# Performance work log

Hardware: AMD Instinct MI355X
Metric: run time of the kernel (lower is better)

The kernel has to match this reference:

```python
import jax, jax.numpy as jnp
import numpy as np
from jax import lax

VOCAB = 18
EMB = 200
HID = 200
SEQ = 128
BATCH = 2048
PAD_IDX = 0


def setup_inputs() -> dict:
    key = jax.random.key(0)
    ks = jax.random.split(key, 8)
    s_emb = 1.0  # torch nn.Embedding default N(0,1)
    s_lstm = 1.0 / np.sqrt(HID)  # torch LSTM default U(-1/sqrt(H), 1/sqrt(H))
    s_lin = 1.0 / np.sqrt(HID)
    inp = {
        "x": jax.random.randint(ks[0], (BATCH, SEQ), 0, VOCAB, dtype=jnp.int32),
        "E": jax.random.normal(ks[1], (VOCAB, EMB), dtype=jnp.float32) * s_emb,
        "W_ih": jax.random.uniform(ks[2], (4 * HID, EMB), minval=-s_lstm, maxval=s_lstm, dtype=jnp.float32),
        "W_hh": jax.random.uniform(ks[3], (4 * HID, HID), minval=-s_lstm, maxval=s_lstm, dtype=jnp.float32),
        "b_ih": jax.random.uniform(ks[4], (4 * HID,), minval=-s_lstm, maxval=s_lstm, dtype=jnp.float32),
        "b_hh": jax.random.uniform(ks[5], (4 * HID,), minval=-s_lstm, maxval=s_lstm, dtype=jnp.float32),
        "W_out": jax.random.uniform(ks[6], (VOCAB, HID), minval=-s_lin, maxval=s_lin, dtype=jnp.float32),
        "b_out": jax.random.uniform(ks[7], (VOCAB,), minval=-s_lin, maxval=s_lin, dtype=jnp.float32),
    }
    return inp


def _forward(x, E, W_ih, W_hh, b_ih, b_hh, W_out, b_out):
    # Embedding with padding_idx=0 (row 0 is zero, no grad flows to it)
    pad_mask = (jnp.arange(VOCAB) != PAD_IDX).astype(E.dtype)[:, None]
    emb = (E * pad_mask)[x]  # (B, T, EMB)
    B = emb.shape[0]
    # Precompute input contribution to all gates for every timestep
    x_proj = jnp.einsum("bte,ge->btg", emb, W_ih) + b_ih + b_hh  # (B, T, 4H)

    def step(carry, xg_t):
        h, c = carry
        gates = xg_t + h @ W_hh.T  # (B, 4H)
        i, f, g, o = jnp.split(gates, 4, axis=-1)  # torch gate order i,f,g,o
        i = jax.nn.sigmoid(i)
        f = jax.nn.sigmoid(f)
        g = jnp.tanh(g)
        o = jax.nn.sigmoid(o)
        c = f * c + i * g
        h = o * jnp.tanh(c)
        return (h, c), h

    h0 = jnp.zeros((B, HID), dtype=emb.dtype)
    c0 = jnp.zeros((B, HID), dtype=emb.dtype)
    (h_n, c_n), hs = lax.scan(step, (h0, c0), x_proj.transpose(1, 0, 2))
    out = hs.transpose(1, 0, 2)  # (B, T, HID)
    logits = out @ W_out.T + b_out  # (B, T, VOCAB)
    return logits, h_n, c_n


def reference(x, E, W_ih, W_hh, b_ih, b_hh, W_out, b_out):
    return _forward(x, E, W_ih, W_hh, b_ih, b_hh, W_out, b_out)
```

## Files before the change

kernel.cpp:

```cpp
#include <hip/hip_runtime.h>

#define VOCAB 18
#define EMB   200
#define HID   200
#define G4    800
#define SEQ   128
#define BATCH 2048
#define MB    8
#define NT    56
#define KS    7
#define TPB   256
#define TPW   14
#define SV    (SEQ*VOCAB)
#define LOGITS_N ((size_t)BATCH*SEQ*VOCAB)

typedef short s16x8 __attribute__((ext_vector_type(8)));
typedef float f32x4 __attribute__((ext_vector_type(4)));

__device__ __forceinline__ unsigned short f2bf(float f) {
  unsigned int u = __float_as_uint(f);
  u += 0x7FFFu + ((u >> 16) & 1u);
  return (unsigned short)(u >> 16);
}
__device__ __forceinline__ float sigm(float x) {
  float e = __builtin_amdgcn_exp2f(x * 1.4426950408889634f);
  return e * __builtin_amdgcn_rcpf(e + 1.0f);
}
__device__ __forceinline__ float tanhq(float x) {
  float e = __builtin_amdgcn_exp2f(x * 2.8853900817779268f);
  return 1.0f - 2.0f * __builtin_amdgcn_rcpf(e + 1.0f);
}

__global__ void prep_tbl(const float* __restrict__ E, const float* __restrict__ W_ih,
                         const float* __restrict__ b_ih, const float* __restrict__ b_hh,
                         unsigned short* __restrict__ tbl) {
  int tid = blockIdx.x * 256 + threadIdx.x;
  if (tid >= VOCAB * G4) return;
  int v = tid / G4, col = tid % G4;
  float s = b_ih[col] + b_hh[col];
  if (v != 0) {
    const float* Er = E + v * EMB;
    const float* Wr = W_ih + col * EMB;
    for (int e = 0; e < EMB; ++e) s += Er[e] * Wr[e];
  }
  tbl[tid] = f2bf(s);
}

__global__ void prep_wp(const float* __restrict__ W_hh, const float* __restrict__ W_out,
                        const float* __restrict__ b_out,
                        const unsigned short* __restrict__ tbl,
                        short* __restrict__ Wp) {
  int u = blockIdx.x * 256 + threadIdx.x;
  if (u >= NT * KS * 64) return;
  int n    = u / (KS * 64);
  int rem  = u % (KS * 64);
  int s_   = rem >> 6;
  int lane = rem & 63;
  int c    = lane & 15;
  int kb   = lane >> 4;
  s16x8 o;
  #pragma unroll
  for (int i = 0; i < 8; ++i) {
    int k = 32 * s_ + 8 * kb + i;
    short b = 0;
    if (n < 50) {
      int g = c & 3, j = 4 * n + (c >> 2);
      int colg = g * 200 + j;
      if (k < HID)                          b = (short)f2bf(W_hh[colg * HID + k]);
      else if (k >= 201 && k < 201 + VOCAB) b = (short)tbl[(k - 201) * G4 + colg];
    } else if (n < 52) {
      int v = 16 * (n - 50) + c;
      if (v < VOCAB) {
        if (k < HID)       b = (short)f2bf(W_out[v * HID + k]);
        else if (k == HID) b = (short)f2bf(b_out[v]);
      }
    }
    o[i] = b;
  }
  *(s16x8*)(Wp + (size_t)u * 8) = o;
}

__global__ __launch_bounds__(TPB) __attribute__((amdgpu_waves_per_eu(1, 1)))
void lstm_kernel(const int* __restrict__ x, const short* __restrict__ Wp,
                 float* __restrict__ out) {
  __shared__ unsigned short hA[KS * 64 * 8];
  __shared__ int   xtok[MB * SEQ];
  __shared__ float logL[MB * SV];
  __shared__ float scr[4][2][8 * 36];

  const int tid  = threadIdx.x;
  const int lane = tid & 63;
  const int w    = tid >> 6;
  const int blk  = blockIdx.x;

  const int wbase = (lane >> 4) * 144 + ((lane & 15) >> 2) * 4 + (lane & 3);
  const int rbase = (lane >> 3) * 36 + (lane & 7) * 4;
  const int jw = 56 * w;

  for (int i = tid; i < KS * 64 * 8; i += TPB)
    hA[i] = (i >= 3200 && i < 3264 && (i & 7) == 0) ? (unsigned short)0x3F80
                                                    : (unsigned short)0;
  for (int i = tid; i < MB * SEQ; i += TPB) xtok[i] = x[blk * (MB * SEQ) + i];

  s16x8 wf[TPW][KS];
  #pragma unroll
  for (int n = 0; n < TPW; ++n) {
    #pragma unroll
    for (int s = 0; s < KS; ++s) {
      wf[n][s] = *(const s16x8*)(Wp + ((((w * TPW + n) * KS) + s) * 64 + lane) * 8);
      asm volatile("" : "+a"(wf[n][s]));
    }
    asm volatile("" ::: "memory");
  }

  float creg[7] = {0.f, 0.f, 0.f, 0.f, 0.f, 0.f, 0.f};
  __syncthreads();

#define DO_PAIR(P, CC) {                                                          \
    f32x4 aA = {0.f,0.f,0.f,0.f}, aB = {0.f,0.f,0.f,0.f};                         \
    _Pragma("unroll")                                                             \
    for (int s = 0; s < KS; ++s) {                                                \
      aA = __builtin_amdgcn_mfma_f32_16x16x32_bf16(aF[s], wf[2*(P)][s],   aA, 0,0,0); \
      aB = __builtin_amdgcn_mfma_f32_16x16x32_bf16(aF[s], wf[2*(P)+1][s], aB, 0,0,0); \
    }                                                                             \
    float* sc = &scr[w][(P) & 1][0];                                              \
    if (lane < 32) {                                                              \
      float* sw = sc + wbase;                                                     \
      sw[0]  = aA[0]; sw[36] = aA[1]; sw[72] = aA[2]; sw[108] = aA[3];            \
      sw[16] = aB[0]; sw[52] = aB[1]; sw[88] = aB[2]; sw[124] = aB[3];            \
    }                                                                             \
    f32x4 gt = *(const f32x4*)(sc + rbase);                                       \
    float i_ = sigm(gt[0]);                                                       \
    float f_ = sigm(gt[1]);                                                       \
    float g_ = tanhq(gt[2]);                                                      \
    float o_ = sigm(gt[3]);                                                       \
    float cn = f_ * (CC) + i_ * g_;                                               \
    float h  = o_ * tanhq(cn);                                                    \
    (CC) = cn;                                                                    \
    int j = jw + 8 * (P) + (lane & 7);                                            \
    hA[((j >> 5) * 64 + 16 * ((j >> 3) & 3) + (lane >> 3)) * 8 + (j & 7)] = f2bf(h); \
    if (t == SEQ - 1) {                                                           \
      size_t bg = (size_t)blk * MB + (lane >> 3);                                 \
      out[LOGITS_N + bg * HID + j] = h;                                           \
      out[LOGITS_N + (size_t)BATCH * HID + bg * HID + j] = cn;                    \
    }                                                                             \
  }

  #pragma unroll 1
  for (int t = 0; t < SEQ; ++t) {
    s16x8 aF[KS];
    #pragma unroll
    for (int s = 0; s < KS; ++s) aF[s] = *(const s16x8*)&hA[(s * 64 + lane) * 8];
    {
      int vv = xtok[(lane & 7) * SEQ + t];
      int js = (lane & 8) ? 100 : (vv + 9 - 8 * (lane >> 4));
      s16x8 a6 = aF[6];
      #pragma unroll
      for (int e = 0; e < 8; ++e)
        a6[e] = (e == js) ? (short)0x3F80 : a6[e];
      aF[6] = a6;
    }

    if (w < 3) {
      DO_PAIR(0, creg[0]); DO_PAIR(1, creg[1]); DO_PAIR(2, creg[2]);
      DO_PAIR(3, creg[3]); DO_PAIR(4, creg[4]); DO_PAIR(5, creg[5]);
      DO_PAIR(6, creg[6]);
    } else {
      DO_PAIR(0, creg[0]); DO_PAIR(1, creg[1]);
      DO_PAIR(2, creg[2]); DO_PAIR(3, creg[3]);
      f32x4 a1 = {0.f,0.f,0.f,0.f}, a2 = {0.f,0.f,0.f,0.f};
      #pragma unroll
      for (int s = 0; s < KS; ++s) {
        a1 = __builtin_amdgcn_mfma_f32_16x16x32_bf16(aF[s], wf[8][s], a1, 0, 0, 0);
        a2 = __builtin_amdgcn_mfma_f32_16x16x32_bf16(aF[s], wf[9][s], a2, 0, 0, 0);
      }
      if (t > 0 && lane < 32) {
        int qrow = (lane >> 4) * 4, c = lane & 15;
        #pragma unroll
        for (int q = 0; q < 4; ++q) {
          if (c < VOCAB)      logL[(qrow + q) * SV + (t - 1) * VOCAB + c]      = a1[q];
          if (c < VOCAB - 16) logL[(qrow + q) * SV + (t - 1) * VOCAB + 16 + c] = a2[q];
        }
      }
    }
    __syncthreads();
  }

  if (w == 3) {
    s16x8 aE[KS];
    #pragma unroll
    for (int s = 0; s < KS; ++s) aE[s] = *(const s16x8*)&hA[(s * 64 + lane) * 8];
    f32x4 a1 = {0.f,0.f,0.f,0.f}, a2 = {0.f,0.f,0.f,0.f};
    #pragma unroll
    for (int s = 0; s < KS; ++s) {
      a1 = __builtin_amdgcn_mfma_f32_16x16x32_bf16(aE[s], wf[8][s], a1, 0, 0, 0);
      a2 = __builtin_amdgcn_mfma_f32_16x16x32_bf16(aE[s], wf[9][s], a2, 0, 0, 0);
    }
    if (lane < 32) {
      int qrow = (lane >> 4) * 4, c = lane & 15;
      #pragma unroll
      for (int q = 0; q < 4; ++q) {
        int base = (qrow + q) * SV + (SEQ - 1) * VOCAB;
        if (c < VOCAB)      logL[base + c]      = a1[q];
        if (c < VOCAB - 16) logL[base + 16 + c] = a2[q];
      }
    }
  }
  __syncthreads();

  float* dst = out + (size_t)blk * (MB * SV);
  for (int i = tid * 4; i < MB * SV; i += TPB * 4)
    *(f32x4*)&dst[i] = *(const f32x4*)&logL[i];
#undef DO_PAIR
}

extern "C" void kernel_launch(void* const* d_in, const int* in_sizes, int n_in,
                              void* d_out, int out_size, void* d_ws, size_t ws_size,
                              hipStream_t stream) {
  const int*   x     = (const int*)  d_in[0];
  const float* E     = (const float*)d_in[1];
  const float* W_ih  = (const float*)d_in[2];
  const float* W_hh  = (const float*)d_in[3];
  const float* b_ih  = (const float*)d_in[4];
  const float* b_hh  = (const float*)d_in[5];
  const float* W_out = (const float*)d_in[6];
  const float* b_out = (const float*)d_in[7];
  float* out = (float*)d_out;

  unsigned short* tbl = (unsigned short*)d_ws;
  short* Wp = (short*)d_ws + VOCAB * G4;

  prep_tbl<<<(VOCAB * G4 + 255) / 256, 256, 0, stream>>>(E, W_ih, b_ih, b_hh, tbl);
  prep_wp<<<(NT * KS * 64 + 255) / 256, 256, 0, stream>>>(W_hh, W_out, b_out, tbl, Wp);
  lstm_kernel<<<BATCH / MB, TPB, 0, stream>>>(x, Wp, out);
}
```

Measured before the change: 354.8 us.

## Replace LDS gate transpose with DPP shuffles and software-pipeline MFMA with elementwise

Drops the per-pair shared-memory scratch round trip used to regroup the four gate values, and instead does a 4x4 register transpose with DPP quad-permute moves. The MFMA tile pairs are software-pipelined so the next pair's matrix multiplies are issued before the current pair's sigmoid/tanh work. A barrier is added after the hA fragment load so h can be overwritten in the same step. This costs more live accumulator registers and an extra barrier per step, and only half the lanes do the elementwise work.

```diff
diff --git a/kernel.cpp b/kernel.cpp
--- a/kernel.cpp
+++ b/kernel.cpp
@@ -29,6 +29,14 @@
 __device__ __forceinline__ float tanhq(float x) {
   float e = __builtin_amdgcn_exp2f(x * 2.8853900817779268f);
   return 1.0f - 2.0f * __builtin_amdgcn_rcpf(e + 1.0f);
+}
+__device__ __forceinline__ float dpp_x1(float v) {
+  return __uint_as_float((unsigned)__builtin_amdgcn_mov_dpp(
+      (int)__float_as_uint(v), 0xB1, 0xF, 0xF, true));
+}
+__device__ __forceinline__ float dpp_x2(float v) {
+  return __uint_as_float((unsigned)__builtin_amdgcn_mov_dpp(
+      (int)__float_as_uint(v), 0x4E, 0xF, 0xF, true));
 }
 
 __global__ void prep_tbl(const float* __restrict__ E, const float* __restrict__ W_ih,
@@ -86,16 +94,15 @@
   __shared__ unsigned short hA[KS * 64 * 8];
   __shared__ int   xtok[MB * SEQ];
   __shared__ float logL[MB * SV];
-  __shared__ float scr[4][2][8 * 36];
 
   const int tid  = threadIdx.x;
   const int lane = tid & 63;
   const int w    = tid >> 6;
   const int blk  = blockIdx.x;
-
-  const int wbase = (lane >> 4) * 144 + ((lane & 15) >> 2) * 4 + (lane & 3);
-  const int rbase = (lane >> 3) * 36 + (lane & 7) * 4;
-  const int jw = 56 * w;
+  const int jw   = 56 * w;
+  const int jj   = (lane >> 2) & 3;
+  const int row  = 4 * ((lane >> 4) & 3) + (lane & 3);
+  const bool pb0 = lane & 1, pb1 = lane & 2;
 
   for (int i = tid; i < KS * 64 * 8; i += TPB)
     hA[i] = (i >= 3200 && i < 3264 && (i & 7) == 0) ? (unsigned short)0x3F80
@@ -113,38 +120,53 @@
     asm volatile("" ::: "memory");
   }
 
-  float creg[7] = {0.f, 0.f, 0.f, 0.f, 0.f, 0.f, 0.f};
+  float cA[7] = {0,0,0,0,0,0,0}, cB[7] = {0,0,0,0,0,0,0};
+  const f32x4 zz = {0.f, 0.f, 0.f, 0.f};
   __syncthreads();
 
-#define DO_PAIR(P, CC) {                                                          \
-    f32x4 aA = {0.f,0.f,0.f,0.f}, aB = {0.f,0.f,0.f,0.f};                         \
-    _Pragma("unroll")                                                             \
-    for (int s = 0; s < KS; ++s) {                                                \
-      aA = __builtin_amdgcn_mfma_f32_16x16x32_bf16(aF[s], wf[2*(P)][s],   aA, 0,0,0); \
-      aB = __builtin_amdgcn_mfma_f32_16x16x32_bf16(aF[s], wf[2*(P)+1][s], aB, 0,0,0); \
-    }                                                                             \
-    float* sc = &scr[w][(P) & 1][0];                                              \
-    if (lane < 32) {                                                              \
-      float* sw = sc + wbase;                                                     \
-      sw[0]  = aA[0]; sw[36] = aA[1]; sw[72] = aA[2]; sw[108] = aA[3];            \
-      sw[16] = aB[0]; sw[52] = aB[1]; sw[88] = aB[2]; sw[124] = aB[3];            \
-    }                                                                             \
-    f32x4 gt = *(const f32x4*)(sc + rbase);                                       \
-    float i_ = sigm(gt[0]);                                                       \
-    float f_ = sigm(gt[1]);                                                       \
-    float g_ = tanhq(gt[2]);                                                      \
-    float o_ = sigm(gt[3]);                                                       \
-    float cn = f_ * (CC) + i_ * g_;                                               \
-    float h  = o_ * tanhq(cn);                                                    \
-    (CC) = cn;                                                                    \
-    int j = jw + 8 * (P) + (lane & 7);                                            \
-    hA[((j >> 5) * 64 + 16 * ((j >> 3) & 3) + (lane >> 3)) * 8 + (j & 7)] = f2bf(h); \
-    if (t == SEQ - 1) {                                                           \
-      size_t bg = (size_t)blk * MB + (lane >> 3);                                 \
-      out[LOGITS_N + bg * HID + j] = h;                                           \
-      out[LOGITS_N + (size_t)BATCH * HID + bg * HID + j] = cn;                    \
-    }                                                                             \
-  }
+#define MFMA_PAIR(nt, A, B) {                                                   \
+    _Pragma("unroll")                                                           \
+    for (int s = 0; s < KS; ++s) {                                              \
+      A = __builtin_amdgcn_mfma_f32_16x16x32_bf16(aF[s], wf[nt][s],     A, 0,0,0); \
+      B = __builtin_amdgcn_mfma_f32_16x16x32_bf16(aF[s], wf[(nt)+1][s], B, 0,0,0); \
+    } }
+
+#define TRANS4(v) {                                                             \
+    float t0 = dpp_x1(v[0]), t1 = dpp_x1(v[1]), t2 = dpp_x1(v[2]), t3 = dpp_x1(v[3]); \
+    v[0] = pb0 ? t1 : v[0];  v[1] = pb0 ? v[1] : t0;                            \
+    v[2] = pb0 ? t3 : v[2];  v[3] = pb0 ? v[3] : t2;                            \
+    t0 = dpp_x2(v[0]); t1 = dpp_x2(v[1]); t2 = dpp_x2(v[2]); t3 = dpp_x2(v[3]); \
+    v[0] = pb1 ? t2 : v[0];  v[1] = pb1 ? t3 : v[1];                            \
+    v[2] = pb1 ? v[2] : t0;  v[3] = pb1 ? v[3] : t1; }
+
+#define EWONE(V, CC, J) {                                                       \
+    float i_ = sigm(V[0]), f_ = sigm(V[1]), g_ = tanhq(V[2]), o_ = sigm(V[3]);  \
+    float cn = f_ * (CC) + i_ * g_;                                             \
+    float h  = o_ * tanhq(cn);                                                  \
+    (CC) = cn;                                                                  \
+    hA[(((J) >> 5) * 64 + 16 * (((J) >> 3) & 3) + row) * 8 + ((J) & 7)] = f2bf(h); \
+    if (t == SEQ - 1) {                                                         \
+      size_t bg = (size_t)blk * MB + row;                                       \
+      out[LOGITS_N + bg * HID + (J)] = h;                                       \
+      out[LOGITS_N + (size_t)BATCH * HID + bg * HID + (J)] = cn;                \
+    } }
+
+#define EW_PAIR(P, A, B) {                                                      \
+    TRANS4(A); TRANS4(B);                                                       \
+    if (lane < 32) {                                                            \
+      int jA = jw + 8 * (P) + jj;                                               \
+      EWONE(A, cA[P], jA);                                                      \
+      EWONE(B, cB[P], jA + 4);                                                  \
+    } }
+
+#define LOGIT_STORE(A, B)                                                       \
+    if (t > 0 && lane < 32) {                                                   \
+      int qrow = (lane >> 4) * 4, c = lane & 15;                                \
+      _Pragma("unroll")                                                         \
+      for (int q = 0; q < 4; ++q) {                                             \
+        logL[(qrow + q) * SV + (t - 1) * VOCAB + c] = A[q];                     \
+        if (c < 2) logL[(qrow + q) * SV + (t - 1) * VOCAB + 16 + c] = B[q];     \
+      } }
 
   #pragma unroll 1
   for (int t = 0; t < SEQ; ++t) {
@@ -160,49 +182,51 @@
         a6[e] = (e == js) ? (short)0x3F80 : a6[e];
       aF[6] = a6;
     }
+    __syncthreads();
 
     if (w < 3) {
-      DO_PAIR(0, creg[0]); DO_PAIR(1, creg[1]); DO_PAIR(2, creg[2]);
-      DO_PAIR(3, creg[3]); DO_PAIR(4, creg[4]); DO_PAIR(5, creg[5]);
-      DO_PAIR(6, creg[6]);
+      f32x4 A0 = zz, B0 = zz, A1 = zz, B1 = zz;
+      MFMA_PAIR(0, A0, B0);
+      MFMA_PAIR(2, A1, B1);   EW_PAIR(0, A0, B0);
+      A0 = zz; B0 = zz;
+      MFMA_PAIR(4, A0, B0);   EW_PAIR(1, A1, B1);
+      A1 = zz; B1 = zz;
+      MFMA_PAIR(6, A1, B1);   EW_PAIR(2, A0, B0);
+      A0 = zz; B0 = zz;
+      MFMA_PAIR(8, A0, B0);   EW_PAIR(3, A1, B1);
+      A1 = zz; B1 = zz;
+      MFMA_PAIR(10, A1, B1);  EW_PAIR(4, A0, B0);
+      A0 = zz; B0 = zz;
+      MFMA_PAIR(12, A0, B0);  EW_PAIR(5, A1, B1);
+      EW_PAIR(6, A0, B0);
     } else {
-      DO_PAIR(0, creg[0]); DO_PAIR(1, creg[1]);
-      DO_PAIR(2, creg[2]); DO_PAIR(3, creg[3]);
-      f32x4 a1 = {0.f,0.f,0.f,0.f}, a2 = {0.f,0.f,0.f,0.f};
-      #pragma unroll
-      for (int s = 0; s < KS; ++s) {
-        a1 = __builtin_amdgcn_mfma_f32_16x16x32_bf16(aF[s], wf[8][s], a1, 0, 0, 0);
-        a2 = __builtin_amdgcn_mfma_f32_16x16x32_bf16(aF[s], wf[9][s], a2, 0, 0, 0);
-      }
-      if (t > 0 && lane < 32) {
-        int qrow = (lane >> 4) * 4, c = lane & 15;
-        #pragma unroll
-        for (int q = 0; q < 4; ++q) {
-          if (c < VOCAB)      logL[(qrow + q) * SV + (t - 1) * VOCAB + c]      = a1[q];
-          if (c < VOCAB - 16) logL[(qrow + q) * SV + (t - 1) * VOCAB + 16 + c] = a2[q];
-        }
-      }
+      f32x4 A0 = zz, B0 = zz, A1 = zz, B1 = zz;
+      MFMA_PAIR(0, A0, B0);
+      MFMA_PAIR(2, A1, B1);   EW_PAIR(0, A0, B0);
+      A0 = zz; B0 = zz;
+      MFMA_PAIR(4, A0, B0);   EW_PAIR(1, A1, B1);
+      A1 = zz; B1 = zz;
+      MFMA_PAIR(6, A1, B1);   EW_PAIR(2, A0, B0);
+      A0 = zz; B0 = zz;
+      MFMA_PAIR(8, A0, B0);   EW_PAIR(3, A1, B1);
+      LOGIT_STORE(A0, B0);
     }
     __syncthreads();
   }
 
   if (w == 3) {
-    s16x8 aE[KS];
+    s16x8 aF[KS];
     #pragma unroll
-    for (int s = 0; s < KS; ++s) aE[s] = *(const s16x8*)&hA[(s * 64 + lane) * 8];
-    f32x4 a1 = {0.f,0.f,0.f,0.f}, a2 = {0.f,0.f,0.f,0.f};
-    #pragma unroll
-    for (int s = 0; s < KS; ++s) {
-      a1 = __builtin_amdgcn_mfma_f32_16x16x32_bf16(aE[s], wf[8][s], a1, 0, 0, 0);
-      a2 = __builtin_amdgcn_mfma_f32_16x16x32_bf16(aE[s], wf[9][s], a2, 0, 0, 0);
-    }
+    for (int s = 0; s < KS; ++s) aF[s] = *(const s16x8*)&hA[(s * 64 + lane) * 8];
+    f32x4 A0 = zz, B0 = zz;
+    MFMA_PAIR(8, A0, B0);
     if (lane < 32) {
       int qrow = (lane >> 4) * 4, c = lane & 15;
       #pragma unroll
       for (int q = 0; q < 4; ++q) {
         int base = (qrow + q) * SV + (SEQ - 1) * VOCAB;
-        if (c < VOCAB)      logL[base + c]      = a1[q];
-        if (c < VOCAB - 16) logL[base + 16 + c] = a2[q];
+        logL[base + c] = A0[q];
+        if (c < 2) logL[base + 16 + c] = B0[q];
       }
     }
   }
@@ -211,7 +235,12 @@
   float* dst = out + (size_t)blk * (MB * SV);
   for (int i = tid * 4; i < MB * SV; i += TPB * 4)
     *(f32x4*)&dst[i] = *(const f32x4*)&logL[i];
-#undef DO_PAIR
+
+#undef MFMA_PAIR
+#undef TRANS4
+#undef EWONE
+#undef EW_PAIR
+#undef LOGIT_STORE
 }
 
 extern "C" void kernel_launch(void* const* d_in, const int* in_sizes, int n_in,
```

New measurement: 426.4 us. +20.2%, slower.
